# Optimization experiments

Hardware: AMD Instinct MI355X
Metric: run time of the kernel (lower is better)

Reference implementation:

```python
import jax, jax.numpy as jnp
import numpy as np

B, T, DIM, HEADS, KV_HEADS = 2, 2048, 1024, 16, 4
HD = DIM // HEADS  # 64


def _rope(t, sin, cos):
    # interleaved RoPE: pairs (2i, 2i+1) rotated by the same angle
    rot = jnp.stack([-t[..., 1::2], t[..., ::2]], axis=-1).reshape(t.shape)
    return t * cos + rot * sin


def setup_inputs() -> dict:
    key = jax.random.key(0)
    kx, kq, kk, kv, ko = jax.random.split(key, 5)
    x = jax.random.normal(kx, (B, T, DIM), dtype=jnp.float32)
    # standard RoPE tables, [T, HD]
    pos = jnp.arange(T, dtype=jnp.float32)
    inv_freq = 1.0 / (10000.0 ** (jnp.arange(0, HD, 2, dtype=jnp.float32) / HD))
    ang = pos[:, None] * inv_freq[None, :]  # [T, HD/2]
    sin = jnp.repeat(jnp.sin(ang), 2, axis=-1)  # [T, HD]
    cos = jnp.repeat(jnp.cos(ang), 2, axis=-1)
    mask = jnp.ones((B, 1, T), dtype=jnp.float32)  # padding mask (all valid)
    s = 1.0 / np.sqrt(DIM).astype(np.float32)
    Wq = jax.random.normal(kq, (DIM, DIM), dtype=jnp.float32) * s
    Wk = jax.random.normal(kk, (DIM, KV_HEADS * HD), dtype=jnp.float32) * s
    Wv = jax.random.normal(kv, (DIM, KV_HEADS * HD), dtype=jnp.float32) * s
    Wo = jax.random.normal(ko, (DIM, DIM), dtype=jnp.float32) * s
    return {"x": x, "sin": sin, "cos": cos, "mask": mask,
            "Wq": Wq, "Wk": Wk, "Wv": Wv, "Wo": Wo}


def reference(x, sin, cos, mask, Wq, Wk, Wv, Wo):
    Bx, Tx, C = x.shape
    # projections -> [B, H, T, HD] / [B, KV, T, HD]
    q = (x @ Wq).reshape(Bx, Tx, HEADS, HD).transpose(0, 2, 1, 3)
    k = (x @ Wk).reshape(Bx, Tx, KV_HEADS, HD).transpose(0, 2, 1, 3)
    v = (x @ Wv).reshape(Bx, Tx, KV_HEADS, HD).transpose(0, 2, 1, 3)
    # RoPE (sin/cos [T, HD] broadcast over batch/heads)
    q = _rope(q, sin, cos)
    k = _rope(k, sin, cos)
    # GQA: expand kv heads to query heads
    groups = HEADS // KV_HEADS
    k = jnp.repeat(k, groups, axis=1)
    v = jnp.repeat(v, groups, axis=1)
    scores = jnp.einsum('bhqd,bhkd->bhqk', q, k) / np.sqrt(HD).astype(np.float32)
    causal = jnp.tril(jnp.ones((Tx, Tx), dtype=bool))  # [T, T]
    m = (mask[:, None, :, :] > 0) & causal  # [B,1,1,T] & [T,T] -> [B,1,T,T]
    scores = jnp.where(m, scores, jnp.asarray(-1e9, scores.dtype))
    attn = jax.nn.softmax(scores, axis=-1)
    out = jnp.einsum('bhqk,bhkd->bhqd', attn, v)
    out = out.transpose(0, 2, 1, 3).reshape(Bx, Tx, C)
    return out @ Wo
```

## Files before the change

kernel.cpp:

```cpp
#include <hip/hip_runtime.h>
#include <math.h>

typedef __attribute__((ext_vector_type(8))) short bf16x8;
typedef __attribute__((ext_vector_type(4))) float f32x4;
typedef __attribute__((ext_vector_type(4))) unsigned short u16x4;

#define B_    2
#define T_    2048
#define DIM_  1024
#define H_    16
#define KV_   4
#define HD_   64

#define QSCALE 0.1803368801111437f
#define SOFF  24.0f

static __device__ __forceinline__ unsigned short f2bf(float f) {
    union { float f; unsigned int u; } v; v.f = f;
    unsigned int r = v.u + 0x7fff + ((v.u >> 16) & 1);
    return (unsigned short)(r >> 16);
}

static __device__ __forceinline__ unsigned int pkbf(float lo, float hi) {
    union { float f; unsigned int u; } a, b; a.f = lo; b.f = hi;
    return ((a.u + 0x8000u) >> 16) | ((b.u + 0x8000u) & 0xffff0000u);
}

static __device__ __forceinline__ void gload16(const void* g, void* l) {
    __builtin_amdgcn_global_load_lds(
        (const __attribute__((address_space(1))) unsigned int*)g,
        (__attribute__((address_space(3))) unsigned int*)l, 16, 0, 0);
}

#define MFMA16(a, b, c) __builtin_amdgcn_mfma_f32_16x16x32_bf16(a, b, c, 0, 0, 0)

#define XB_OFF   0u
#define WT_OFF   4194304u
#define WOT_OFF  5767168u
#define QB_OFF   6815744u
#define KB_OFF   11010048u
#define VTB_OFF  12058624u
#define AB_OFF   13107200u
#define MB_OFF   17301504u

static __device__ __forceinline__ void wtrans_body(
    const float* __restrict__ W, unsigned short* __restrict__ Wt, int N,
    int n0, int k0, int tid, float (*Ts)[65])
{
    const int r = tid >> 4, c4 = (tid & 15) * 4;
    #pragma unroll
    for (int i = 0; i < 4; ++i) {
        float4 v = *(const float4*)&W[(size_t)(k0 + r + 16 * i) * N + n0 + c4];
        Ts[r + 16 * i][c4 + 0] = v.x; Ts[r + 16 * i][c4 + 1] = v.y;
        Ts[r + 16 * i][c4 + 2] = v.z; Ts[r + 16 * i][c4 + 3] = v.w;
    }
    __syncthreads();
    const int rn = tid >> 3, ck = (tid & 7) * 8;
    #pragma unroll
    for (int i = 0; i < 2; ++i) {
        int n = rn + 32 * i;
        unsigned short u[8];
        #pragma unroll
        for (int e = 0; e < 8; ++e) u[e] = f2bf(Ts[ck + e][n]);
        *(bf16x8*)&Wt[(size_t)(n0 + n) * 1024 + k0 + ck] = *(bf16x8*)u;
    }
}

__global__ __launch_bounds__(256) void prepass_kernel(
    const float* __restrict__ x,
    const float* __restrict__ Wq, const float* __restrict__ Wk,
    const float* __restrict__ Wv, const float* __restrict__ Wo,
    const float* __restrict__ maskp,
    unsigned short* __restrict__ xb, unsigned short* __restrict__ Wt,
    unsigned short* __restrict__ Wot, float* __restrict__ mbias)
{
    __shared__ float Ts[64][65];
    const int blk = blockIdx.x, tid = threadIdx.x;

    if (blk < 2048) {
        const size_t i = ((size_t)blk * 256 + tid) * 8;
        float4 a = *(const float4*)&x[i];
        float4 b = *(const float4*)&x[i + 4];
        unsigned short u[8] = {f2bf(a.x), f2bf(a.y), f2bf(a.z), f2bf(a.w),
                               f2bf(b.x), f2bf(b.y), f2bf(b.z), f2bf(b.w)};
        *(bf16x8*)&xb[i] = *(bf16x8*)u;
    } else if (blk < 2304) {
        const int sb = blk - 2048;
        wtrans_body(Wq, Wt, 1024, (sb & 15) * 64, (sb >> 4) * 64, tid, Ts);
    } else if (blk < 2368) {
        const int sb = blk - 2304;
        wtrans_body(Wk, Wt + 1024u * 1024u, 256, (sb & 3) * 64, (sb >> 2) * 64,
                    tid, Ts);
    } else if (blk < 2432) {
        const int sb = blk - 2368;
        wtrans_body(Wv, Wt + 1280u * 1024u, 256, (sb & 3) * 64, (sb >> 2) * 64,
                    tid, Ts);
    } else if (blk < 2688) {
        const int sb = blk - 2432;
        wtrans_body(Wo, Wot, 1024, (sb & 15) * 64, (sb >> 4) * 64, tid, Ts);
    } else {
        #pragma unroll
        for (int e = 0; e < 4; ++e) {
            const int i = tid * 16 + e * 4;
            f32x4 mv = *(const f32x4*)&maskp[i];
            f32x4 bv;
            #pragma unroll
            for (int j = 0; j < 4; ++j) bv[j] = mv[j] > 0.f ? -SOFF : -1e30f;
            *(f32x4*)&mbias[i] = bv;
        }
    }
}

__global__ __launch_bounds__(256) void qkv_mfma_kernel(
    const unsigned short* __restrict__ xb, const unsigned short* __restrict__ Wt,
    const float* __restrict__ sinp, const float* __restrict__ cosp,
    unsigned short* __restrict__ Qw, unsigned short* __restrict__ Kw,
    unsigned short* __restrict__ Vtw)
{
    __shared__ __align__(16) unsigned char As[8192];
    __shared__ __align__(16) unsigned char Bs[16384];

    const int tid = threadIdx.x, lane = tid & 63, w = tid >> 6;
    const int lr = lane & 15, lg = lane >> 4;
    const int wm = w >> 1, wn = w & 1;
    const int bn = blockIdx.x, bm = blockIdx.y;
    const int m0 = bm * 64, n0 = bn * 128;

    const int chunkR = lane >> 3;
    const int srcOff = 8 * ((lane & 7) ^ chunkR);

    f32x4 acc[2][4] = {};

    for (int k0 = 0; k0 < 1024; k0 += 64) {
        __syncthreads();
        #pragma unroll
        for (int i = 0; i < 6; ++i) {
            const int c = w * 6 + i;
            if (c < 8) {
                const int row = c * 8 + chunkR;
                gload16(xb + (size_t)(m0 + row) * 1024 + k0 + srcOff, As + c * 1024);
            } else {
                const int row = (c - 8) * 8 + chunkR;
                gload16(Wt + (size_t)(n0 + row) * 1024 + k0 + srcOff,
                        Bs + (c - 8) * 1024);
            }
        }
        __syncthreads();
        #pragma unroll
        for (int kk = 0; kk < 2; ++kk) {
            bf16x8 af[2], bfr[4];
            #pragma unroll
            for (int mf = 0; mf < 2; ++mf) {
                const int row = wm * 32 + mf * 16 + lr;
                af[mf] = *(const bf16x8*)(As + row * 128 +
                          ((kk * 64 + lg * 16) ^ ((row & 7) << 4)));
            }
            #pragma unroll
            for (int nf = 0; nf < 4; ++nf) {
                const int row = wn * 64 + nf * 16 + lr;
                bfr[nf] = *(const bf16x8*)(Bs + row * 128 +
                          ((kk * 64 + lg * 16) ^ ((row & 7) << 4)));
            }
            #pragma unroll
            for (int mf = 0; mf < 2; ++mf)
                #pragma unroll
                for (int nf = 0; nf < 4; ++nf)
                    acc[mf][nf] = MFMA16(af[mf], bfr[nf], acc[mf][nf]);
        }
    }

    const float rsign = (lane & 1) ? 1.f : -1.f;
    #pragma unroll
    for (int nf = 0; nf < 4; ++nf) {
        const int col = n0 + wn * 64 + nf * 16 + lr;
        #pragma unroll
        for (int mf = 0; mf < 2; ++mf) {
            const int mrow = m0 + wm * 32 + mf * 16 + lg * 4;
            const int b = mrow >> 11;
            const int t0 = mrow & 2047;
            if (col < 1280) {
                const int d = col & 63;
                #pragma unroll
                for (int r = 0; r < 4; ++r) {
                    float val = acc[mf][nf][r];
                    float partner = __shfl_xor(val, 1);
                    const int t = t0 + r;
                    float cs = cosp[t * 64 + d], sn = sinp[t * 64 + d];
                    float rv = val * cs + rsign * partner * sn;
                    if (col < 1024) {
                        const int h = col >> 6;
                        Qw[(((size_t)b * H_ + h) * T_ + t) * 64 + d] =
                            f2bf(rv * QSCALE);
                    } else {
                        const int kv = (col - 1024) >> 6;
                        char* krow = (char*)Kw +
                            ((((size_t)b * KV_ + kv) * T_ + t) << 7);
                        *(unsigned short*)(krow + ((2 * d) ^ ((t & 7) << 4))) =
                            f2bf(rv);
                    }
                }
            } else {
                const int cv = col - 1280, kv = cv >> 6, d = cv & 63;
                unsigned short u[4];
                #pragma unroll
                for (int r = 0; r < 4; ++r) u[r] = f2bf(acc[mf][nf][r]);
                char* vrow = (char*)Vtw +
                    ((((size_t)b * KV_ + kv) * 64 + d) * (size_t)T_ * 2);
                *(u16x4*)(vrow + ((2 * t0) ^ ((d & 7) << 4))) = *(u16x4*)u;
            }
        }
    }
}

__global__ __launch_bounds__(512, 4) void attn_kernel(
    const unsigned short* __restrict__ Qg, const unsigned short* __restrict__ Kg,
    const unsigned short* __restrict__ Vtg, const float* __restrict__ mbias,
    unsigned short* __restrict__ attn_out)
{
    __shared__ __align__(16) unsigned char Kl[2][8192];
    __shared__ __align__(16) unsigned char Vl[2][8192];
    __shared__ __align__(16) unsigned char Pl[16384];
    __shared__ float Lb[256];

    const int tid  = threadIdx.x;
    const int lane = tid & 63;
    const int w    = tid >> 6;
    const int grp  = w >> 2;
    const int wq   = w & 3;
    const int lr   = lane & 15;
    const int lg   = lane >> 4;

    const int bi   = blockIdx.x;
    const int qt   = 31 - (bi >> 5);
    const int bh   = bi & 31;
    const int h    = bh & 15;
    const int b    = bh >> 4;
    const int kvh  = h >> 2;
    const int q0   = qt * 64;
    const int qrow = q0 + wq * 16 + lr;

    const int nt    = qt + 1;
    const int mid   = nt >> 1;
    const int iters = nt - mid;

    const char* Kb = (const char*)(Kg  + ((size_t)b * KV_ + kvh) * T_ * HD_);
    const char* Vb = (const char*)(Vtg + ((size_t)b * KV_ + kvh) * HD_ * T_);
    const float* brow = mbias + b * T_;

    const int sr  = lane >> 3;
    const int scb = (lane & 7) * 16;
    unsigned char* Pw = &Pl[w * 2048];

    const unsigned short* Qbase =
        Qg + (((size_t)b * H_ + h) * T_ + qrow) * HD_;
    const bf16x8 qf0 = *(const bf16x8*)(Qbase + lg * 8);
    const bf16x8 qf1 = *(const bf16x8*)(Qbase + 32 + lg * 8);

    f32x4 o[4] = {};
    float l = 0.f;

    for (int it = 0; it < iters; ++it) {
        const int ktg = grp ? (mid + it) : it;
        const bool active = grp || (it < mid);
        const int k0 = ktg * 64;

        if (active) {
            #pragma unroll
            for (int i = 0; i < 2; ++i) {
                const int rb  = wq * 2 + i;
                const int row = rb * 8 + sr;
                gload16(Kb + (size_t)(k0 + row) * 128 + scb, &Kl[grp][rb * 1024]);
                gload16(Vb + (size_t)row * 4096 + 2 * k0 + scb, &Vl[grp][rb * 1024]);
            }
        }
        __syncthreads();

        if (active) {
            const unsigned char* Kc = Kl[grp];
            const unsigned char* Vc = Vl[grp];

            f32x4 bv[4];
            #pragma unroll
            for (int n = 0; n < 4; ++n)
                bv[n] = *(const f32x4*)&brow[k0 + 16 * n + 4 * lg];

            f32x4 s[4] = {};
            __builtin_amdgcn_s_setprio(1);
            #pragma unroll
            for (int n = 0; n < 4; ++n) {
                const int key = 16 * n + lr;
                #pragma unroll
                for (int ks = 0; ks < 2; ++ks) {
                    bf16x8 kb = *(const bf16x8*)(Kc +
                        ((key * 128 + 64 * ks + lg * 16) ^ ((key & 7) << 4)));
                    s[n] = MFMA16(kb, ks == 0 ? qf0 : qf1, s[n]);
                }
            }
            __builtin_amdgcn_s_setprio(0);

            if (ktg == qt) {
                #pragma unroll
                for (int n = 0; n < 4; ++n)
                    #pragma unroll
                    for (int r = 0; r < 4; ++r) {
                        const int keyg = k0 + 16 * n + 4 * lg + r;
                        s[n][r] = (keyg <= qrow) ? s[n][r] + bv[n][r] : -1e30f;
                    }
            } else {
                #pragma unroll
                for (int n = 0; n < 4; ++n)
                    #pragma unroll
                    for (int r = 0; r < 4; ++r) s[n][r] += bv[n][r];
            }
            #pragma unroll
            for (int n = 0; n < 4; ++n)
                #pragma unroll
                for (int r = 0; r < 4; ++r)
                    s[n][r] = exp2f(s[n][r]);

            float tsum[4];
            #pragma unroll
            for (int n = 0; n < 4; ++n)
                tsum[n] = (s[n][0] + s[n][1]) + (s[n][2] + s[n][3]);
            l += (tsum[0] + tsum[1]) + (tsum[2] + tsum[3]);

            #pragma unroll
            for (int n = 0; n < 4; ++n) {
                uint2 wv;
                wv.x = pkbf(s[n][0], s[n][1]);
                wv.y = pkbf(s[n][2], s[n][3]);
                *(uint2*)(Pw + ((lr * 128 + 32 * n + 8 * lg) ^ ((lr & 7) << 4))) = wv;
            }
            bf16x8 pa0 = *(const bf16x8*)(Pw + ((lr * 128 +      lg * 16) ^ ((lr & 7) << 4)));
            bf16x8 pa1 = *(const bf16x8*)(Pw + ((lr * 128 + 64 + lg * 16) ^ ((lr & 7) << 4)));

            __builtin_amdgcn_s_setprio(1);
            #pragma unroll
            for (int n = 0; n < 4; ++n) {
                const int d = 16 * n + lr;
                #pragma unroll
                for (int ks = 0; ks < 2; ++ks) {
                    bf16x8 vb = *(const bf16x8*)(Vc +
                        ((d * 128 + 64 * ks + lg * 16) ^ ((d & 7) << 4)));
                    o[n] = MFMA16(vb, ks == 0 ? pa0 : pa1, o[n]);
                }
            }
            __builtin_amdgcn_s_setprio(0);
        }

        __syncthreads();
    }

    const int slot = wq * 64 + lane;
    if (grp) {
        float* ob = (float*)Pl;
        #pragma unroll
        for (int n = 0; n < 4; ++n)
            *(f32x4*)&ob[slot * 16 + n * 4] = o[n];
        Lb[slot] = l;
    }
    __syncthreads();
    if (!grp) {
        const float* ob = (const float*)Pl;
        #pragma unroll
        for (int n = 0; n < 4; ++n) {
            f32x4 obv = *(const f32x4*)&ob[slot * 16 + n * 4];
            o[n] += obv;
        }
        float lf = l + Lb[slot];
        lf += __shfl_xor(lf, 16);
        lf += __shfl_xor(lf, 32);
        const float linv = 1.f / lf;
        unsigned short* orow =
            attn_out + ((size_t)b * T_ + qrow) * DIM_ + h * HD_;
        #pragma unroll
        for (int n = 0; n < 4; ++n) {
            unsigned short u[4];
            #pragma unroll
            for (int r = 0; r < 4; ++r) u[r] = f2bf(o[n][r] * linv);
            *(u16x4*)&orow[16 * n + 4 * lg] = *(u16x4*)u;
        }
    }
}

__global__ __launch_bounds__(256) void outproj_mfma_kernel(
    const unsigned short* __restrict__ Ab, const unsigned short* __restrict__ Wot,
    float* __restrict__ out)
{
    __shared__ __align__(16) unsigned char As[8192];
    __shared__ __align__(16) unsigned char Bs[16384];

    const int tid = threadIdx.x, lane = tid & 63, w = tid >> 6;
    const int lr = lane & 15, lg = lane >> 4;
    const int wm = w >> 1, wn = w & 1;
    const int bn = blockIdx.x, bm = blockIdx.y;
    const int m0 = bm * 64, n0 = bn * 128;

    const int chunkR = lane >> 3;
    const int srcOff = 8 * ((lane & 7) ^ chunkR);

    f32x4 acc[2][4] = {};

    for (int k0 = 0; k0 < 1024; k0 += 64) {
        __syncthreads();
        #pragma unroll
        for (int i = 0; i < 6; ++i) {
            const int c = w * 6 + i;
            if (c < 8) {
                const int row = c * 8 + chunkR;
                gload16(Ab + (size_t)(m0 + row) * 1024 + k0 + srcOff, As + c * 1024);
            } else {
                const int row = (c - 8) * 8 + chunkR;
                gload16(Wot + (size_t)(n0 + row) * 1024 + k0 + srcOff,
                        Bs + (c - 8) * 1024);
            }
        }
        __syncthreads();
        #pragma unroll
        for (int kk = 0; kk < 2; ++kk) {
            bf16x8 af[2], bfr[4];
            #pragma unroll
            for (int mf = 0; mf < 2; ++mf) {
                const int row = wm * 32 + mf * 16 + lr;
                af[mf] = *(const bf16x8*)(As + row * 128 +
                          ((kk * 64 + lg * 16) ^ ((row & 7) << 4)));
            }
            #pragma unroll
            for (int nf = 0; nf < 4; ++nf) {
                const int row = wn * 64 + nf * 16 + lr;
                bfr[nf] = *(const bf16x8*)(Bs + row * 128 +
                          ((kk * 64 + lg * 16) ^ ((row & 7) << 4)));
            }
            #pragma unroll
            for (int mf = 0; mf < 2; ++mf)
                #pragma unroll
                for (int nf = 0; nf < 4; ++nf)
                    acc[mf][nf] = MFMA16(af[mf], bfr[nf], acc[mf][nf]);
        }
    }

    #pragma unroll
    for (int nf = 0; nf < 4; ++nf) {
        const int col = n0 + wn * 64 + nf * 16 + lr;
        #pragma unroll
        for (int mf = 0; mf < 2; ++mf) {
            const int mrow = m0 + wm * 32 + mf * 16 + lg * 4;
            #pragma unroll
            for (int r = 0; r < 4; ++r)
                out[(size_t)(mrow + r) * 1024 + col] = acc[mf][nf][r];
        }
    }
}

extern "C" void kernel_launch(void* const* d_in, const int* in_sizes, int n_in,
                              void* d_out, int out_size, void* d_ws, size_t ws_size,
                              hipStream_t stream)
{
    const float* x     = (const float*)d_in[0];
    const float* sinp  = (const float*)d_in[1];
    const float* cosp  = (const float*)d_in[2];
    const float* maskp = (const float*)d_in[3];
    const float* Wq    = (const float*)d_in[4];
    const float* Wk    = (const float*)d_in[5];
    const float* Wv    = (const float*)d_in[6];
    const float* Wo    = (const float*)d_in[7];

    unsigned short* wsb = (unsigned short*)d_ws;
    unsigned short* xb  = wsb + XB_OFF;
    unsigned short* Wt  = wsb + WT_OFF;
    unsigned short* Wot = wsb + WOT_OFF;
    unsigned short* Qw  = wsb + QB_OFF;
    unsigned short* Kw  = wsb + KB_OFF;
    unsigned short* Vtw = wsb + VTB_OFF;
    unsigned short* Ab  = wsb + AB_OFF;
    float* mbias        = (float*)(wsb + MB_OFF);
    float* out = (float*)d_out;

    prepass_kernel<<<2689, 256, 0, stream>>>(x, Wq, Wk, Wv, Wo, maskp,
                                             xb, Wt, Wot, mbias);
    qkv_mfma_kernel<<<dim3(12, 64), 256, 0, stream>>>(xb, Wt, sinp, cosp,
                                                      Qw, Kw, Vtw);
    attn_kernel<<<dim3(1024), 512, 0, stream>>>(
        Qw, Kw, Vtw, mbias, Ab);
    outproj_mfma_kernel<<<dim3(8, 64), 256, 0, stream>>>(Ab, Wot, out);
}
```

Baseline: 103.9 us.

## Pair query tiles per block so each K/V tile feeds two query tiles

Each attention block now handles two adjacent 64-row query tiles (2pg and 2pg+1) instead of one, halving the grid to 512 blocks. The two wave groups split the key range evenly (pg+1 tiles each), which removes the idle iterations in the old uneven causal split, and every K/V tile loaded into LDS is reused for both query tiles. The cost is twice the accumulators and score registers per wave, a reused P buffer that is written and read twice per iteration, and fewer blocks to spread across CUs.

```diff
diff --git a/kernel.cpp b/kernel.cpp
--- a/kernel.cpp
+++ b/kernel.cpp
@@ -219,8 +219,8 @@
 {
     __shared__ __align__(16) unsigned char Kl[2][8192];
     __shared__ __align__(16) unsigned char Vl[2][8192];
-    __shared__ __align__(16) unsigned char Pl[16384];
-    __shared__ float Lb[256];
+    __shared__ __align__(16) unsigned char Pl[8][2048];
+    __shared__ float Lb[512];
 
     const int tid  = threadIdx.x;
     const int lane = tid & 63;
@@ -231,17 +231,17 @@
     const int lg   = lane >> 4;
 
     const int bi   = blockIdx.x;
-    const int qt   = 31 - (bi >> 5);
+    const int pg   = 15 - (bi >> 5);
     const int bh   = bi & 31;
     const int h    = bh & 15;
     const int b    = bh >> 4;
     const int kvh  = h >> 2;
-    const int q0   = qt * 64;
-    const int qrow = q0 + wq * 16 + lr;
-
-    const int nt    = qt + 1;
-    const int mid   = nt >> 1;
-    const int iters = nt - mid;
+    const int qa_t = 2 * pg;
+    const int qb_t = 2 * pg + 1;
+    const int qra  = qa_t * 64 + wq * 16 + lr;
+    const int qrb  = qra + 64;
+
+    const int iters = pg + 1;
 
     const char* Kb = (const char*)(Kg  + ((size_t)b * KV_ + kvh) * T_ * HD_);
     const char* Vb = (const char*)(Vtg + ((size_t)b * KV_ + kvh) * HD_ * T_);
@@ -249,91 +249,109 @@
 
     const int sr  = lane >> 3;
     const int scb = (lane & 7) * 16;
-    unsigned char* Pw = &Pl[w * 2048];
-
-    const unsigned short* Qbase =
-        Qg + (((size_t)b * H_ + h) * T_ + qrow) * HD_;
-    const bf16x8 qf0 = *(const bf16x8*)(Qbase + lg * 8);
-    const bf16x8 qf1 = *(const bf16x8*)(Qbase + 32 + lg * 8);
-
-    f32x4 o[4] = {};
-    float l = 0.f;
+    unsigned char* Pw = &Pl[w][0];
+
+    const unsigned short* Qba = Qg + (((size_t)b * H_ + h) * T_ + qra) * HD_;
+    const unsigned short* Qbb = Qg + (((size_t)b * H_ + h) * T_ + qrb) * HD_;
+    const bf16x8 qfa0 = *(const bf16x8*)(Qba + lg * 8);
+    const bf16x8 qfa1 = *(const bf16x8*)(Qba + 32 + lg * 8);
+    const bf16x8 qfb0 = *(const bf16x8*)(Qbb + lg * 8);
+    const bf16x8 qfb1 = *(const bf16x8*)(Qbb + 32 + lg * 8);
+
+    f32x4 oa[4] = {}, ob[4] = {};
+    float la = 0.f, lb = 0.f;
 
     for (int it = 0; it < iters; ++it) {
-        const int ktg = grp ? (mid + it) : it;
-        const bool active = grp || (it < mid);
-        const int k0 = ktg * 64;
-
-        if (active) {
-            #pragma unroll
-            for (int i = 0; i < 2; ++i) {
-                const int rb  = wq * 2 + i;
-                const int row = rb * 8 + sr;
-                gload16(Kb + (size_t)(k0 + row) * 128 + scb, &Kl[grp][rb * 1024]);
-                gload16(Vb + (size_t)row * 4096 + 2 * k0 + scb, &Vl[grp][rb * 1024]);
-            }
+        const int ktg = grp ? (pg + 1 + it) : it;
+        const int k0  = ktg * 64;
+
+        #pragma unroll
+        for (int i = 0; i < 2; ++i) {
+            const int rb  = wq * 2 + i;
+            const int row = rb * 8 + sr;
+            gload16(Kb + (size_t)(k0 + row) * 128 + scb, &Kl[grp][rb * 1024]);
+            gload16(Vb + (size_t)row * 4096 + 2 * k0 + scb, &Vl[grp][rb * 1024]);
         }
         __syncthreads();
 
-        if (active) {
-            const unsigned char* Kc = Kl[grp];
-            const unsigned char* Vc = Vl[grp];
-
-            f32x4 bv[4];
+        const unsigned char* Kc = Kl[grp];
+        const unsigned char* Vc = Vl[grp];
+
+        f32x4 bv[4];
+        #pragma unroll
+        for (int n = 0; n < 4; ++n)
+            bv[n] = *(const f32x4*)&brow[k0 + 16 * n + 4 * lg];
+
+        f32x4 sa[4] = {}, sb[4] = {};
+        __builtin_amdgcn_s_setprio(1);
+        #pragma unroll
+        for (int n = 0; n < 4; ++n) {
+            const int key = 16 * n + lr;
+            #pragma unroll
+            for (int ks = 0; ks < 2; ++ks) {
+                bf16x8 kb = *(const bf16x8*)(Kc +
+                    ((key * 128 + 64 * ks + lg * 16) ^ ((key & 7) << 4)));
+                sa[n] = MFMA16(kb, ks == 0 ? qfa0 : qfa1, sa[n]);
+                sb[n] = MFMA16(kb, ks == 0 ? qfb0 : qfb1, sb[n]);
+            }
+        }
+        __builtin_amdgcn_s_setprio(0);
+
+        if (ktg >= qa_t) {
             #pragma unroll
             for (int n = 0; n < 4; ++n)
-                bv[n] = *(const f32x4*)&brow[k0 + 16 * n + 4 * lg];
-
-            f32x4 s[4] = {};
-            __builtin_amdgcn_s_setprio(1);
-            #pragma unroll
-            for (int n = 0; n < 4; ++n) {
-                const int key = 16 * n + lr;
-                #pragma unroll
-                for (int ks = 0; ks < 2; ++ks) {
-                    bf16x8 kb = *(const bf16x8*)(Kc +
-                        ((key * 128 + 64 * ks + lg * 16) ^ ((key & 7) << 4)));
-                    s[n] = MFMA16(kb, ks == 0 ? qf0 : qf1, s[n]);
+                #pragma unroll
+                for (int r = 0; r < 4; ++r) {
+                    const int keyg = k0 + 16 * n + 4 * lg + r;
+                    sa[n][r] = (keyg <= qra) ? sa[n][r] + bv[n][r] : -1e30f;
                 }
-            }
-            __builtin_amdgcn_s_setprio(0);
-
-            if (ktg == qt) {
-                #pragma unroll
-                for (int n = 0; n < 4; ++n)
-                    #pragma unroll
-                    for (int r = 0; r < 4; ++r) {
-                        const int keyg = k0 + 16 * n + 4 * lg + r;
-                        s[n][r] = (keyg <= qrow) ? s[n][r] + bv[n][r] : -1e30f;
-                    }
-            } else {
-                #pragma unroll
-                for (int n = 0; n < 4; ++n)
-                    #pragma unroll
-                    for (int r = 0; r < 4; ++r) s[n][r] += bv[n][r];
-            }
+        } else {
             #pragma unroll
             for (int n = 0; n < 4; ++n)
                 #pragma unroll
-                for (int r = 0; r < 4; ++r)
-                    s[n][r] = exp2f(s[n][r]);
-
-            float tsum[4];
+                for (int r = 0; r < 4; ++r) sa[n][r] += bv[n][r];
+        }
+        if (ktg == qb_t) {
             #pragma unroll
             for (int n = 0; n < 4; ++n)
-                tsum[n] = (s[n][0] + s[n][1]) + (s[n][2] + s[n][3]);
-            l += (tsum[0] + tsum[1]) + (tsum[2] + tsum[3]);
-
-            #pragma unroll
-            for (int n = 0; n < 4; ++n) {
-                uint2 wv;
-                wv.x = pkbf(s[n][0], s[n][1]);
-                wv.y = pkbf(s[n][2], s[n][3]);
-                *(uint2*)(Pw + ((lr * 128 + 32 * n + 8 * lg) ^ ((lr & 7) << 4))) = wv;
-            }
+                #pragma unroll
+                for (int r = 0; r < 4; ++r) {
+                    const int keyg = k0 + 16 * n + 4 * lg + r;
+                    sb[n][r] = (keyg <= qrb) ? sb[n][r] + bv[n][r] : -1e30f;
+                }
+        } else {
+            #pragma unroll
+            for (int n = 0; n < 4; ++n)
+                #pragma unroll
+                for (int r = 0; r < 4; ++r) sb[n][r] += bv[n][r];
+        }
+        #pragma unroll
+        for (int n = 0; n < 4; ++n)
+            #pragma unroll
+            for (int r = 0; r < 4; ++r) {
+                sa[n][r] = exp2f(sa[n][r]);
+                sb[n][r] = exp2f(sb[n][r]);
+            }
+
+        float ta[4], tb[4];
+        #pragma unroll
+        for (int n = 0; n < 4; ++n) {
+            ta[n] = (sa[n][0] + sa[n][1]) + (sa[n][2] + sa[n][3]);
+            tb[n] = (sb[n][0] + sb[n][1]) + (sb[n][2] + sb[n][3]);
+        }
+        la += (ta[0] + ta[1]) + (ta[2] + ta[3]);
+        lb += (tb[0] + tb[1]) + (tb[2] + tb[3]);
+
+        #pragma unroll
+        for (int n = 0; n < 4; ++n) {
+            uint2 wv;
+            wv.x = pkbf(sa[n][0], sa[n][1]);
+            wv.y = pkbf(sa[n][2], sa[n][3]);
+            *(uint2*)(Pw + ((lr * 128 + 32 * n + 8 * lg) ^ ((lr & 7) << 4))) = wv;
+        }
+        {
             bf16x8 pa0 = *(const bf16x8*)(Pw + ((lr * 128 +      lg * 16) ^ ((lr & 7) << 4)));
             bf16x8 pa1 = *(const bf16x8*)(Pw + ((lr * 128 + 64 + lg * 16) ^ ((lr & 7) << 4)));
-
             __builtin_amdgcn_s_setprio(1);
             #pragma unroll
             for (int n = 0; n < 4; ++n) {
@@ -342,7 +360,31 @@
                 for (int ks = 0; ks < 2; ++ks) {
                     bf16x8 vb = *(const bf16x8*)(Vc +
                         ((d * 128 + 64 * ks + lg * 16) ^ ((d & 7) << 4)));
-                    o[n] = MFMA16(vb, ks == 0 ? pa0 : pa1, o[n]);
+                    oa[n] = MFMA16(vb, ks == 0 ? pa0 : pa1, oa[n]);
+                }
+            }
+            __builtin_amdgcn_s_setprio(0);
+        }
+
+        #pragma unroll
+        for (int n = 0; n < 4; ++n) {
+            uint2 wv;
+            wv.x = pkbf(sb[n][0], sb[n][1]);
+            wv.y = pkbf(sb[n][2], sb[n][3]);
+            *(uint2*)(Pw + ((lr * 128 + 32 * n + 8 * lg) ^ ((lr & 7) << 4))) = wv;
+        }
+        {
+            bf16x8 pb0 = *(const bf16x8*)(Pw + ((lr * 128 +      lg * 16) ^ ((lr & 7) << 4)));
+            bf16x8 pb1 = *(const bf16x8*)(Pw + ((lr * 128 + 64 + lg * 16) ^ ((lr & 7) << 4)));
+            __builtin_amdgcn_s_setprio(1);
+            #pragma unroll
+            for (int n = 0; n < 4; ++n) {
+                const int d = 16 * n + lr;
+                #pragma unroll
+                for (int ks = 0; ks < 2; ++ks) {
+                    bf16x8 vb = *(const bf16x8*)(Vc +
+                        ((d * 128 + 64 * ks + lg * 16) ^ ((d & 7) << 4)));
+                    ob[n] = MFMA16(vb, ks == 0 ? pb0 : pb1, ob[n]);
                 }
             }
             __builtin_amdgcn_s_setprio(0);
@@ -353,32 +395,45 @@
 
     const int slot = wq * 64 + lane;
     if (grp) {
-        float* ob = (float*)Pl;
-        #pragma unroll
-        for (int n = 0; n < 4; ++n)
-            *(f32x4*)&ob[slot * 16 + n * 4] = o[n];
-        Lb[slot] = l;
+        float* pa = (float*)Kl;
+        float* pb = (float*)Vl;
+        #pragma unroll
+        for (int n = 0; n < 4; ++n) {
+            *(f32x4*)&pa[slot * 16 + n * 4] = oa[n];
+            *(f32x4*)&pb[slot * 16 + n * 4] = ob[n];
+        }
+        Lb[slot]       = la;
+        Lb[256 + slot] = lb;
     }
     __syncthreads();
     if (!grp) {
-        const float* ob = (const float*)Pl;
-        #pragma unroll
-        for (int n = 0; n < 4; ++n) {
-            f32x4 obv = *(const f32x4*)&ob[slot * 16 + n * 4];
-            o[n] += obv;
-        }
-        float lf = l + Lb[slot];
-        lf += __shfl_xor(lf, 16);
-        lf += __shfl_xor(lf, 32);
-        const float linv = 1.f / lf;
-        unsigned short* orow =
-            attn_out + ((size_t)b * T_ + qrow) * DIM_ + h * HD_;
-        #pragma unroll
-        for (int n = 0; n < 4; ++n) {
-            unsigned short u[4];
-            #pragma unroll
-            for (int r = 0; r < 4; ++r) u[r] = f2bf(o[n][r] * linv);
-            *(u16x4*)&orow[16 * n + 4 * lg] = *(u16x4*)u;
+        const float* pa = (const float*)Kl;
+        const float* pb = (const float*)Vl;
+        #pragma unroll
+        for (int n = 0; n < 4; ++n) {
+            oa[n] += *(const f32x4*)&pa[slot * 16 + n * 4];
+            ob[n] += *(const f32x4*)&pb[slot * 16 + n * 4];
+        }
+        float lfa = la + Lb[slot];
+        float lfb = lb + Lb[256 + slot];
+        lfa += __shfl_xor(lfa, 16);
+        lfa += __shfl_xor(lfa, 32);
+        lfb += __shfl_xor(lfb, 16);
+        lfb += __shfl_xor(lfb, 32);
+        const float lia = 1.f / lfa;
+        const float lib = 1.f / lfb;
+        unsigned short* ra = attn_out + ((size_t)b * T_ + qra) * DIM_ + h * HD_;
+        unsigned short* rb = attn_out + ((size_t)b * T_ + qrb) * DIM_ + h * HD_;
+        #pragma unroll
+        for (int n = 0; n < 4; ++n) {
+            unsigned short ua[4], ub[4];
+            #pragma unroll
+            for (int r = 0; r < 4; ++r) {
+                ua[r] = f2bf(oa[n][r] * lia);
+                ub[r] = f2bf(ob[n][r] * lib);
+            }
+            *(u16x4*)&ra[16 * n + 4 * lg] = *(u16x4*)ua;
+            *(u16x4*)&rb[16 * n + 4 * lg] = *(u16x4*)ub;
         }
     }
 }
@@ -480,7 +535,7 @@
                                              xb, Wt, Wot, mbias);
     qkv_mfma_kernel<<<dim3(12, 64), 256, 0, stream>>>(xb, Wt, sinp, cosp,
                                                       Qw, Kw, Vtw);
-    attn_kernel<<<dim3(1024), 512, 0, stream>>>(
+    attn_kernel<<<dim3(512), 512, 0, stream>>>(
         Qw, Kw, Vtw, mbias, Ab);
     outproj_mfma_kernel<<<dim3(8, 64), 256, 0, stream>>>(Ab, Wot, out);
 }
```

After: 190.6 us. 83.5% more time.
